# Kernel tuning notes

Measured on AMD Instinct MI355X. Metric: run time of the kernel, lower is better.

Reference implementation:

```python
import jax, jax.numpy as jnp
import numpy as np

H2 = 128  # 2*hidden_dim

def setup_inputs() -> dict:
    key = jax.random.key(0)
    k1, k2, k3 = jax.random.split(key, 3)
    B, Lb, Lp = 64, 1024, 1024
    body = jax.random.normal(k1, (B, Lb, H2), dtype=jnp.float32)
    pun = jax.random.normal(k2, (B, Lp, H2), dtype=jnp.float32)
    w_u = jax.random.normal(k3, (3 * H2, 1), dtype=jnp.float32)
    return {"batch_size": B, "body": body, "pun": pun, "w_u": w_u}

def reference(batch_size, body, pun, w_u):
    # score[b,i,j] = [body_i ; pun_j ; body_i*pun_j] @ w_u
    # Decompose w_u into the three 128-dim blocks so the double loop fuses
    # into two matvecs plus one weighted batched GEMM.
    w = w_u[:, 0]
    w1, w2, w3 = w[:H2], w[H2:2 * H2], w[2 * H2:]
    s_body = jnp.einsum('bid,d->bi', body, w1)          # [B, Lb]
    s_pun = jnp.einsum('bjd,d->bj', pun, w2)            # [B, Lp]
    s_cross = jnp.einsum('bid,bjd->bij', body * w3, pun)  # [B, Lb, Lp]
    return s_cross + s_body[:, :, None] + s_pun[:, None, :]
```

## Files before the change

kernel.cpp:

```cpp
#include <hip/hip_runtime.h>


#define LSEQ 1024
#define H2K  128


typedef __attribute__((ext_vector_type(8))) short bfrag;
typedef __attribute__((ext_vector_type(4))) float f32x4;

__device__ __forceinline__ short f2bf(float x) {
    unsigned u = __float_as_uint(x);
    unsigned r = (u + 0x7fff + ((u >> 16) & 1)) >> 16;
    return (short)r;
}
__device__ __forceinline__ float bf2f(short s) {
    return __uint_as_float(((unsigned)(unsigned short)s) << 16);
}

__device__ __forceinline__ void ld16(void* lds, const void* g) {
    __builtin_amdgcn_global_load_lds(
        (const __attribute__((address_space(1))) void*)g,
        (__attribute__((address_space(3))) void*)lds, 16, 0, 0);
}

__global__ __launch_bounds__(256) void prep_kernel(
    const float* __restrict__ body, const float* __restrict__ pun,
    const float* __restrict__ w_u, float* __restrict__ ws)
{
    const int flag = blockIdx.y;
    const int lane = threadIdx.x & 63;
    const int wv   = threadIdx.x >> 6;
    const size_t row = (size_t)blockIdx.x * 4 + wv;

    const float* src = (flag ? pun : body) + row * H2K;
    const float2 v  = *(const float2*)(src + lane * 2);
    const float2 wm = *(const float2*)(w_u + flag * H2K + lane * 2);

    float p = v.x * wm.x + v.y * wm.y;
    p += __shfl_xor(p, 32);
    p += __shfl_xor(p, 16);
    p += __shfl_xor(p, 8);
    p += __shfl_xor(p, 4);
    p += __shfl_xor(p, 2);
    p += __shfl_xor(p, 1);
    if (lane == 0) ws[(size_t)flag * 65536 + row] = p;

    float cx = v.x, cy = v.y;
    if (!flag) {
        const float2 w3v = *(const float2*)(w_u + 2 * H2K + lane * 2);
        cx *= w3v.x; cy *= w3v.y;
    }
    const short h0 = f2bf(cx), h1 = f2bf(cy);
    const short l0 = f2bf(cx - bf2f(h0)), l1 = f2bf(cy - bf2f(h1));

    short* hb = (short*)(ws + 131072) + (size_t)flag * 16777216 + row * H2K + lane * 2;
    *(unsigned*)hb =
        ((unsigned)(unsigned short)h0) | ((unsigned)(unsigned short)h1 << 16);
    *(unsigned*)(hb + 8388608) =
        ((unsigned)(unsigned short)l0) | ((unsigned)(unsigned short)l1 << 16);
}

__global__ __launch_bounds__(512, 4) void align_mfma(
    const float* __restrict__ ws, float* __restrict__ out)
{
    __shared__ __align__(16) short Ah[4096], Al[4096], Bh[4096], Bl[4096];

    const int bb = blockIdx.z;
    const int ti = blockIdx.y * 128, tj = blockIdx.x * 128;
    const int t    = threadIdx.x;
    const int lane = t & 63;
    const int w    = t >> 6;

    const int srow = w * 16 + (lane & 15);
    const int k8   = lane >> 4;

    const short* base = (const short*)(ws + 131072);
    const size_t arow = (size_t)(bb * LSEQ + ti + srow) * H2K + k8 * 8;
    const size_t brow = (size_t)(bb * LSEQ + tj + srow) * H2K + k8 * 8;
    const short* pAh = base + arow;
    const short* pAl = base + 8388608 + arow;
    const short* pBh = base + 16777216 + brow;
    const short* pBl = base + 25165824 + brow;

    short* dAh = &Ah[t * 8];
    short* dAl = &Al[t * 8];
    short* dBh = &Bh[t * 8];
    short* dBl = &Bl[t * 8];

    const int mt0 = (w >> 1) * 2;
    const int nt0 = (w & 1) * 4;
    f32x4 acc[2][4] = {};

    for (int kt = 0; kt < 4; ++kt) {
        if (kt) __syncthreads();

        ld16(dAh, pAh + kt * 32);
        ld16(dAl, pAl + kt * 32);
        ld16(dBh, pBh + kt * 32);
        ld16(dBl, pBl + kt * 32);
        __syncthreads();

        bfrag ah[2], al[2], bh[4], bl[4];
#pragma unroll
        for (int i = 0; i < 2; ++i) {
            ah[i] = *(const bfrag*)&Ah[((mt0 + i) * 64 + lane) * 8];
            al[i] = *(const bfrag*)&Al[((mt0 + i) * 64 + lane) * 8];
        }
#pragma unroll
        for (int j = 0; j < 4; ++j) {
            bh[j] = *(const bfrag*)&Bh[((nt0 + j) * 64 + lane) * 8];
            bl[j] = *(const bfrag*)&Bl[((nt0 + j) * 64 + lane) * 8];
        }
#pragma unroll
        for (int i = 0; i < 2; ++i)
#pragma unroll
            for (int j = 0; j < 4; ++j) {
                acc[i][j] = __builtin_amdgcn_mfma_f32_16x16x32_bf16(ah[i], bh[j], acc[i][j], 0, 0, 0);
                acc[i][j] = __builtin_amdgcn_mfma_f32_16x16x32_bf16(ah[i], bl[j], acc[i][j], 0, 0, 0);
                acc[i][j] = __builtin_amdgcn_mfma_f32_16x16x32_bf16(al[i], bh[j], acc[i][j], 0, 0, 0);
            }
    }

    const float* sbp = ws + (size_t)bb * LSEQ;
    const float* spp = ws + 65536 + (size_t)bb * LSEQ;
    const int quad = lane >> 4, ln = lane & 15;
#pragma unroll
    for (int i = 0; i < 2; ++i) {
        const int rbase = ti + (mt0 + i) * 16 + quad * 4;
#pragma unroll
        for (int j = 0; j < 4; ++j) {
            const int col = tj + (nt0 + j) * 16 + ln;
            const float spv = spp[col];
#pragma unroll
            for (int v = 0; v < 4; ++v) {
                const int row = rbase + v;
                out[((size_t)bb * LSEQ + row) * LSEQ + col] = acc[i][j][v] + sbp[row] + spv;
            }
        }
    }
}

extern "C" void kernel_launch(void* const* d_in, const int* in_sizes, int n_in,
                              void* d_out, int out_size, void* d_ws, size_t ws_size,
                              hipStream_t stream) {
    const float* body = (const float*)d_in[1];
    const float* pun  = (const float*)d_in[2];
    const float* w_u  = (const float*)d_in[3];
    float* out = (float*)d_out;
    float* ws  = (float*)d_ws;
    const int B = in_sizes[1] / (LSEQ * H2K);

    dim3 g1((B * LSEQ) / 4, 2, 1);
    prep_kernel<<<g1, 256, 0, stream>>>(body, pun, w_u, ws);

    dim3 g2(LSEQ / 128, LSEQ / 128, B);
    align_mfma<<<g2, 512, 0, stream>>>(ws, out);
}
```

Baseline: 393.6 us.

## Double-buffer LDS tiles and swap operands for vectorized float4 output stores

Adds double-buffered LDS for the body and pun tiles, so the global-to-LDS load of the next k-step is issued before the MFMAs of the current step, with explicit vmcnt waits and raw barriers replacing __syncthreads. It also swaps the MFMA operand roles so each lane's accumulator holds four consecutive output columns. The epilogue can then write float4 stores instead of scalar strided ones. The cost is doubled LDS use (64 KB per block), which may limit occupancy, and hand-written waitcnt logic that is fragile.

```diff
diff --git a/kernel.cpp b/kernel.cpp
--- a/kernel.cpp
+++ b/kernel.cpp
@@ -63,79 +63,89 @@
 __global__ __launch_bounds__(512, 4) void align_mfma(
     const float* __restrict__ ws, float* __restrict__ out)
 {
-    __shared__ __align__(16) short Ah[4096], Al[4096], Bh[4096], Bl[4096];
+    __shared__ __align__(16) short Ch[2][4096], Cl[2][4096];
+    __shared__ __align__(16) short Ph[2][4096], Pl[2][4096];
 
     const int bb = blockIdx.z;
-    const int ti = blockIdx.y * 128, tj = blockIdx.x * 128;
+    const int ti = blockIdx.y * 128;
+    const int tj = blockIdx.x * 128;
     const int t    = threadIdx.x;
     const int lane = t & 63;
     const int w    = t >> 6;
 
     const int srow = w * 16 + (lane & 15);
     const int k8   = lane >> 4;
-
     const short* base = (const short*)(ws + 131072);
-    const size_t arow = (size_t)(bb * LSEQ + ti + srow) * H2K + k8 * 8;
-    const size_t brow = (size_t)(bb * LSEQ + tj + srow) * H2K + k8 * 8;
-    const short* pAh = base + arow;
-    const short* pAl = base + 8388608 + arow;
-    const short* pBh = base + 16777216 + brow;
-    const short* pBl = base + 25165824 + brow;
-
-    short* dAh = &Ah[t * 8];
-    short* dAl = &Al[t * 8];
-    short* dBh = &Bh[t * 8];
-    short* dBl = &Bl[t * 8];
+    const size_t crow = (size_t)(bb * LSEQ + ti + srow) * H2K + k8 * 8;
+    const size_t prow = (size_t)(bb * LSEQ + tj + srow) * H2K + k8 * 8;
+    const short* gCh = base + crow;
+    const short* gCl = base + 8388608 + crow;
+    const short* gPh = base + 16777216 + prow;
+    const short* gPl = base + 25165824 + prow;
 
     const int mt0 = (w >> 1) * 2;
     const int nt0 = (w & 1) * 4;
     f32x4 acc[2][4] = {};
 
+    ld16(&Ch[0][t * 8], gCh);
+    ld16(&Cl[0][t * 8], gCl);
+    ld16(&Ph[0][t * 8], gPh);
+    ld16(&Pl[0][t * 8], gPl);
+
+#pragma unroll
     for (int kt = 0; kt < 4; ++kt) {
-        if (kt) __syncthreads();
+        const int cur = kt & 1, nxt = cur ^ 1;
 
-        ld16(dAh, pAh + kt * 32);
-        ld16(dAl, pAl + kt * 32);
-        ld16(dBh, pBh + kt * 32);
-        ld16(dBl, pBl + kt * 32);
-        __syncthreads();
+        if (kt < 3) {
+            ld16(&Ch[nxt][t * 8], gCh + (kt + 1) * 32);
+            ld16(&Cl[nxt][t * 8], gCl + (kt + 1) * 32);
+            ld16(&Ph[nxt][t * 8], gPh + (kt + 1) * 32);
+            ld16(&Pl[nxt][t * 8], gPl + (kt + 1) * 32);
+        }
+        __builtin_amdgcn_sched_barrier(0);
+        if (kt < 3) asm volatile("s_waitcnt vmcnt(4)" ::: "memory");
+        else        asm volatile("s_waitcnt vmcnt(0)" ::: "memory");
+        __builtin_amdgcn_s_barrier();
 
-        bfrag ah[2], al[2], bh[4], bl[4];
+        bfrag ph[2], pl[2], ch[4], cl[4];
 #pragma unroll
         for (int i = 0; i < 2; ++i) {
-            ah[i] = *(const bfrag*)&Ah[((mt0 + i) * 64 + lane) * 8];
-            al[i] = *(const bfrag*)&Al[((mt0 + i) * 64 + lane) * 8];
+            ph[i] = *(const bfrag*)&Ph[cur][((mt0 + i) * 64 + lane) * 8];
+            pl[i] = *(const bfrag*)&Pl[cur][((mt0 + i) * 64 + lane) * 8];
         }
 #pragma unroll
         for (int j = 0; j < 4; ++j) {
-            bh[j] = *(const bfrag*)&Bh[((nt0 + j) * 64 + lane) * 8];
-            bl[j] = *(const bfrag*)&Bl[((nt0 + j) * 64 + lane) * 8];
+            ch[j] = *(const bfrag*)&Ch[cur][((nt0 + j) * 64 + lane) * 8];
+            cl[j] = *(const bfrag*)&Cl[cur][((nt0 + j) * 64 + lane) * 8];
         }
 #pragma unroll
         for (int i = 0; i < 2; ++i)
 #pragma unroll
             for (int j = 0; j < 4; ++j) {
-                acc[i][j] = __builtin_amdgcn_mfma_f32_16x16x32_bf16(ah[i], bh[j], acc[i][j], 0, 0, 0);
-                acc[i][j] = __builtin_amdgcn_mfma_f32_16x16x32_bf16(ah[i], bl[j], acc[i][j], 0, 0, 0);
-                acc[i][j] = __builtin_amdgcn_mfma_f32_16x16x32_bf16(al[i], bh[j], acc[i][j], 0, 0, 0);
+                acc[i][j] = __builtin_amdgcn_mfma_f32_16x16x32_bf16(ph[i], ch[j], acc[i][j], 0, 0, 0);
+                acc[i][j] = __builtin_amdgcn_mfma_f32_16x16x32_bf16(ph[i], cl[j], acc[i][j], 0, 0, 0);
+                acc[i][j] = __builtin_amdgcn_mfma_f32_16x16x32_bf16(pl[i], ch[j], acc[i][j], 0, 0, 0);
             }
+
+        if (kt < 3) __builtin_amdgcn_s_barrier();
+        __builtin_amdgcn_sched_barrier(0);
     }
 
     const float* sbp = ws + (size_t)bb * LSEQ;
     const float* spp = ws + 65536 + (size_t)bb * LSEQ;
-    const int quad = lane >> 4, ln = lane & 15;
+    const int q = lane >> 4, ln = lane & 15;
 #pragma unroll
-    for (int i = 0; i < 2; ++i) {
-        const int rbase = ti + (mt0 + i) * 16 + quad * 4;
+    for (int mi = 0; mi < 2; ++mi) {
+        const int j0 = tj + (mt0 + mi) * 16 + q * 4;
+        const float4 spv = *(const float4*)(spp + j0);
 #pragma unroll
-        for (int j = 0; j < 4; ++j) {
-            const int col = tj + (nt0 + j) * 16 + ln;
-            const float spv = spp[col];
-#pragma unroll
-            for (int v = 0; v < 4; ++v) {
-                const int row = rbase + v;
-                out[((size_t)bb * LSEQ + row) * LSEQ + col] = acc[i][j][v] + sbp[row] + spv;
-            }
+        for (int ni = 0; ni < 4; ++ni) {
+            const int row = ti + (nt0 + ni) * 16 + ln;
+            const float sb = sbp[row];
+            const f32x4 a = acc[mi][ni];
+            float4 r = { a[0] + sb + spv.x, a[1] + sb + spv.y,
+                         a[2] + sb + spv.z, a[3] + sb + spv.w };
+            *(float4*)&out[((size_t)bb * LSEQ + row) * LSEQ + j0] = r;
         }
     }
 }
```

Result: slower. 402.2 us (+2.2%).
